# Performance work log

Hardware: AMD Instinct MI355X
Metric: run time of the kernel (lower is better)

Reference implementation:

```python
import jax, jax.numpy as jnp
import numpy as np

B, S, R, C_Q, C_KV, H, C_A = 1, 128, 256, 256, 256, 8, 32


def setup_inputs() -> dict:
    key = jax.random.key(0)
    ks = jax.random.split(key, 11)
    scale = 0.02
    q = jax.random.normal(ks[0], (B, S, R, C_Q), jnp.float32)
    kv = jax.random.normal(ks[1], (B, S, R, C_KV), jnp.float32)
    bias = jax.random.normal(ks[2], (B, 1, R, R, H), jnp.float32)
    bias_mask = jax.random.randint(ks[3], (B, S, R), 0, 2).astype(jnp.float32)
    w_q = jax.random.normal(ks[4], (C_Q, H, C_A), jnp.float32) * scale
    w_k = jax.random.normal(ks[5], (C_KV, H, C_A), jnp.float32) * scale
    w_v = jax.random.normal(ks[6], (C_KV, H, C_A), jnp.float32) * scale
    w_g = jax.random.normal(ks[7], (C_Q, H, C_A), jnp.float32) * scale
    b_g = jax.random.normal(ks[8], (H, C_A), jnp.float32) * scale
    w_o = jax.random.normal(ks[9], (H, C_A, C_Q), jnp.float32) * scale
    b_o = jax.random.normal(ks[10], (C_Q,), jnp.float32) * scale
    return {"q": q, "kv": kv, "bias": bias, "bias_mask": bias_mask,
            "w_q": w_q, "w_k": w_k, "w_v": w_v, "w_g": w_g, "b_g": b_g,
            "w_o": w_o, "b_o": b_o}


def reference(q, kv, bias, bias_mask, w_q, w_k, w_v, w_g, b_g, w_o, b_o):
    # q, kv: [B, S, R, C]; attention over residue dim R within each row s.
    c_a = w_q.shape[-1]
    normsize = 1.0 / jnp.sqrt(jnp.asarray(c_a, q.dtype))
    Q = jnp.einsum('bsqc,chd->bsqhd', q, w_q) * normsize  # [B,S,R,H,Ca]
    K = jnp.einsum('bskc,chd->bskhd', kv, w_k)
    V = jnp.einsum('bskc,chd->bskhd', kv, w_v)
    # affinity: [B,S,Q,K,H]
    AT = jnp.einsum('bsqhd,bskhd->bsqkh', Q, K)
    mask_bias = (bias_mask[:, :, None, :, None] - 1.0) * 1e9  # [B,S,1,K,1]
    AT = AT + bias + mask_bias
    AT = jax.nn.softmax(AT, axis=-2)  # softmax over K
    O = jnp.einsum('bsqkh,bskhd->bsqhd', AT, V)
    G = jax.nn.sigmoid(jnp.einsum('bsqc,chd->bsqhd', q, w_g) + b_g)
    O = O * G
    out = jnp.einsum('bsqhd,hdc->bsqc', O, w_o) + b_o  # [B,S,R,C_Q]
    return out
```

## Files before the change

### kernel.cpp

```cpp
#include <hip/hip_runtime.h>

typedef __bf16 bf16;
typedef __bf16 bf16x8 __attribute__((ext_vector_type(8)));
typedef float  f32x4  __attribute__((ext_vector_type(4)));
typedef unsigned int u32;

#define MFMA16(a, b, c) __builtin_amdgcn_mfma_f32_16x16x32_bf16((a), (b), (c), 0, 0, 0)


typedef __attribute__((address_space(3))) u32 lds_u32;
typedef const __attribute__((address_space(1))) u32 glob_u32;
__device__ __forceinline__ void gll16(const void* g, void* l) {
    __builtin_amdgcn_global_load_lds((glob_u32*)g, (lds_u32*)l, 16, 0, 0);
}

__global__ __launch_bounds__(256) void prep_kernel(
    const float* __restrict__ q, const float* __restrict__ kv,
    const float* __restrict__ bias,
    const float* __restrict__ w_q, const float* __restrict__ w_k,
    const float* __restrict__ w_v, const float* __restrict__ w_g,
    const float* __restrict__ w_o,
    bf16* __restrict__ qbf, bf16* __restrict__ kvbf, float* __restrict__ biasT,
    bf16* __restrict__ Wqg, bf16* __restrict__ Wkv, bf16* __restrict__ Wo)
{
    const float norm = 0.17677669529663687f;
    const int gid = blockIdx.x * 256 + threadIdx.x;
    const int gsz = gridDim.x * 256;

    for (int u = gid; u < 2097152; u += gsz) {
        const float* src; bf16* dst;
        if (u < 1048576) { src = q + (size_t)u * 8;            dst = qbf  + (size_t)u * 8; }
        else             { src = kv + (size_t)(u - 1048576)*8; dst = kvbf + (size_t)(u - 1048576)*8; }
        float4 x0 = *(const float4*)(src);
        float4 x1 = *(const float4*)(src + 4);
        bf16x8 t;
        t[0]=(bf16)x0.x; t[1]=(bf16)x0.y; t[2]=(bf16)x0.z; t[3]=(bf16)x0.w;
        t[4]=(bf16)x1.x; t[5]=(bf16)x1.y; t[6]=(bf16)x1.z; t[7]=(bf16)x1.w;
        *(bf16x8*)dst = t;
    }
    for (int u = gid; u < 524288; u += gsz) {
        int h = u >> 16, qq = (u >> 8) & 255, kk = u & 255;
        biasT[u] = bias[(((qq << 8) + kk) << 3) + h];
    }
    for (int u = gid; u < 131072; u += gsz) {
        int n = u >> 8, k = u & 255;
        float v = (n < 256) ? w_q[k * 256 + n] * norm : w_g[k * 256 + (n - 256)];
        Wqg[u] = (bf16)v;
    }
    for (int u = gid; u < 131072; u += gsz) {
        int n = u >> 8, k = u & 255;
        float v = (n < 256) ? w_k[k * 256 + n] : w_v[k * 256 + (n - 256)];
        Wkv[u] = (bf16)v;
    }
    for (int u = gid; u < 65536; u += gsz) {
        int n = u >> 8, k = u & 255;
        Wo[u] = (bf16)w_o[k * 256 + n];
    }
}

template<bool F32OUT>
__device__ __forceinline__ void gemm_core(
    const bf16* __restrict__ A, const bf16* __restrict__ Bw,
    bf16* __restrict__ Cb, float* __restrict__ Cf, const float* __restrict__ bo,
    int m0, int n0, int ntot)
{
    __shared__ __align__(16) bf16 As[128 * 32];
    __shared__ __align__(16) bf16 Bs[128 * 32];

    const int tid  = threadIdx.x;
    const int lane = tid & 63, wave = tid >> 6;
    const int quad = lane >> 4, lc = lane & 15;
    const int wr = wave >> 1, wc = wave & 1;

    const int r0 = tid >> 2, p0 = tid & 3;
    const int c1 = tid + 256;
    const int r1 = (c1 & 255) >> 2, p1 = c1 & 3;
    const bf16* gA0 = A  + (size_t)(m0 + r0) * 256 + p0 * 8;
    const bf16* gA1 = A  + (size_t)(m0 + 64 + r0) * 256 + p0 * 8;
    const bf16* gB0 = Bw + (size_t)(n0 + r0) * 256 + p0 * 8;
    const bf16* gB1 = Bw + (size_t)(n0 + 64 + r0) * 256 + p0 * 8;
    bf16* lA0 = As + tid * 8;
    bf16* lA1 = As + (tid + 256) * 8;
    bf16* lB0 = Bs + tid * 8;
    bf16* lB1 = Bs + (tid + 256) * 8;
    (void)r1; (void)p1;

    f32x4 acc[4][4];
    #pragma unroll
    for (int i = 0; i < 4; ++i)
        #pragma unroll
        for (int j = 0; j < 4; ++j) acc[i][j] = f32x4{0.f, 0.f, 0.f, 0.f};

    #pragma unroll 1
    for (int kb = 0; kb < 8; ++kb) {
        const int ko = kb * 32;
        gll16(gA0 + ko, lA0);
        gll16(gA1 + ko, lA1);
        gll16(gB0 + ko, lB0);
        gll16(gB1 + ko, lB1);
        __syncthreads();

        bf16x8 aF[4], bF[4];
        #pragma unroll
        for (int mt = 0; mt < 4; ++mt)
            aF[mt] = *(const bf16x8*)(As + (wr * 64 + mt * 16 + lc) * 32 + quad * 8);
        #pragma unroll
        for (int nt = 0; nt < 4; ++nt)
            bF[nt] = *(const bf16x8*)(Bs + (wc * 64 + nt * 16 + lc) * 32 + quad * 8);
        #pragma unroll
        for (int mt = 0; mt < 4; ++mt)
            #pragma unroll
            for (int nt = 0; nt < 4; ++nt)
                acc[mt][nt] = MFMA16(aF[mt], bF[nt], acc[mt][nt]);
        __syncthreads();
    }

    #pragma unroll
    for (int mt = 0; mt < 4; ++mt) {
        #pragma unroll
        for (int nt = 0; nt < 4; ++nt) {
            const int row = m0 + wr * 64 + mt * 16 + quad * 4;
            const int col = n0 + wc * 64 + nt * 16 + lc;
            if (F32OUT) {
                float b = bo[col];
                #pragma unroll
                for (int rr = 0; rr < 4; ++rr)
                    Cf[(size_t)(row + rr) * ntot + col] = acc[mt][nt][rr] + b;
            } else {
                #pragma unroll
                for (int rr = 0; rr < 4; ++rr)
                    Cb[(size_t)(row + rr) * ntot + col] = (bf16)acc[mt][nt][rr];
            }
        }
    }
}


__global__ __launch_bounds__(256) void proj_kernel(
    const bf16* __restrict__ qbf, const bf16* __restrict__ kvbf,
    const bf16* __restrict__ Wqg, const bf16* __restrict__ Wkv,
    bf16* __restrict__ QG, bf16* __restrict__ KV)
{
    int bid = blockIdx.x;
    bool sel = bid >= 1024;
    int b = sel ? bid - 1024 : bid;
    int m0 = (b >> 2) * 128, n0 = (b & 3) * 128;
    gemm_core<false>(sel ? kvbf : qbf, sel ? Wkv : Wqg,
                     sel ? KV : QG, nullptr, nullptr, m0, n0, 512);
}

__global__ __launch_bounds__(256) void outproj_kernel(
    const bf16* __restrict__ OG, const bf16* __restrict__ Wo,
    const float* __restrict__ bo, float* __restrict__ out)
{
    int b = blockIdx.x;
    int m0 = (b >> 1) * 128, n0 = (b & 1) * 128;
    gemm_core<true>(OG, Wo, nullptr, out, bo, m0, n0, 256);
}

#define A_OFF_MASK 0
#define A_OFF_K    1024
#define A_OFF_VT   21504
#define A_OFF_P    38400
#define A_LDS_TOT  (38400 + 4 * 16 * 264 * 2)

__global__ __launch_bounds__(256) void attn_kernel(
    const bf16* __restrict__ QG, const bf16* __restrict__ KV,
    const float* __restrict__ biasT, const float* __restrict__ bias_mask,
    const float* __restrict__ b_g, bf16* __restrict__ OG)
{
    __shared__ __align__(16) char smem[A_LDS_TOT];
    float* maskadd = (float*)(smem + A_OFF_MASK);
    bf16*  Ks      = (bf16*)(smem + A_OFF_K);
    bf16*  Vt      = (bf16*)(smem + A_OFF_VT);

    const int tid  = threadIdx.x;
    const int wave = tid >> 6, lane = tid & 63;
    const int quad = lane >> 4, lc = lane & 15;
    const int h = blockIdx.x & 7;
    const int s = blockIdx.x >> 3;

    maskadd[tid] = (bias_mask[s * 256 + tid] - 1.0f) * 1e9f;
    {
        const bf16* kvrow = KV + (size_t)(s * 256 + tid) * 512 + h * 32;
        #pragma unroll
        for (int j = 0; j < 4; ++j)
            *(bf16x8*)(Ks + tid * 40 + j * 8) = *(const bf16x8*)(kvrow + j * 8);
        bf16x8 vx[4];
        #pragma unroll
        for (int j = 0; j < 4; ++j) vx[j] = *(const bf16x8*)(kvrow + 256 + j * 8);
        #pragma unroll
        for (int d = 0; d < 32; ++d)
            Vt[d * 264 + tid] = vx[d >> 3][d & 7];
    }
    __syncthreads();

    bf16* P = (bf16*)(smem + A_OFF_P) + wave * (16 * 264);
    const bf16* qgbase = QG + (size_t)(s * 256) * 512 + h * 32;

    #pragma unroll 1
    for (int p = 0; p < 4; ++p) {
        const int q0 = (wave * 4 + p) * 16;

        bf16x8 qf = *(const bf16x8*)(qgbase + (size_t)(q0 + lc) * 512 + quad * 8);

        f32x4 sc[16];
        #pragma unroll
        for (int kt = 0; kt < 16; ++kt) {
            bf16x8 kf = *(const bf16x8*)(Ks + (kt * 16 + lc) * 40 + quad * 8);
            f32x4 z = {0.f, 0.f, 0.f, 0.f};
            sc[kt] = MFMA16(qf, kf, z);
        }

        const float* bT = biasT + (((size_t)h * 256 + q0 + quad * 4) << 8);
        float sum[4] = {0.f, 0.f, 0.f, 0.f};
        #pragma unroll
        for (int kt = 0; kt < 16; ++kt) {
            float mv = maskadd[kt * 16 + lc];
            #pragma unroll
            for (int rr = 0; rr < 4; ++rr) {
                float e = __expf(sc[kt][rr] + bT[rr * 256 + kt * 16 + lc] + mv);
                sc[kt][rr] = e;
                sum[rr] += e;
            }
        }
        #pragma unroll
        for (int rr = 0; rr < 4; ++rr) {
            #pragma unroll
            for (int off = 8; off; off >>= 1) sum[rr] += __shfl_xor(sum[rr], off, 64);
        }
        float inv[4];
        #pragma unroll
        for (int rr = 0; rr < 4; ++rr) inv[rr] = 1.0f / sum[rr];

        #pragma unroll
        for (int kt = 0; kt < 16; ++kt)
            #pragma unroll
            for (int rr = 0; rr < 4; ++rr)
                P[(quad * 4 + rr) * 264 + kt * 16 + lc] = (bf16)(sc[kt][rr] * inv[rr]);

        f32x4 o0 = {0.f,0.f,0.f,0.f}, o1 = {0.f,0.f,0.f,0.f};
        #pragma unroll
        for (int ks = 0; ks < 8; ++ks) {
            bf16x8 pf = *(const bf16x8*)(P + lc * 264 + ks * 32 + quad * 8);
            bf16x8 v0 = *(const bf16x8*)(Vt + lc * 264 + ks * 32 + quad * 8);
            bf16x8 v1 = *(const bf16x8*)(Vt + (16 + lc) * 264 + ks * 32 + quad * 8);
            o0 = MFMA16(pf, v0, o0);
            o1 = MFMA16(pf, v1, o1);
        }

        const bf16* gbase = QG + (size_t)(s * 256) * 512 + 256 + h * 32;
        size_t obase = ((size_t)(s * 256 + q0 + quad * 4)) * 256 + h * 32;
        #pragma unroll
        for (int nt = 0; nt < 2; ++nt) {
            f32x4 ov = nt ? o1 : o0;
            float bg = b_g[h * 32 + nt * 16 + lc];
            #pragma unroll
            for (int rr = 0; rr < 4; ++rr) {
                float gp = (float)gbase[(size_t)(q0 + quad * 4 + rr) * 512 + nt * 16 + lc] + bg;
                float g = 1.0f / (1.0f + __expf(-gp));
                OG[obase + (size_t)rr * 256 + nt * 16 + lc] = (bf16)(ov[rr] * g);
            }
        }
    }
}

extern "C" void kernel_launch(void* const* d_in, const int* in_sizes, int n_in,
                              void* d_out, int out_size, void* d_ws, size_t ws_size,
                              hipStream_t stream)
{
    (void)in_sizes; (void)n_in; (void)out_size; (void)ws_size;
    const float* q    = (const float*)d_in[0];
    const float* kv   = (const float*)d_in[1];
    const float* bias = (const float*)d_in[2];
    const float* mask = (const float*)d_in[3];
    const float* w_q  = (const float*)d_in[4];
    const float* w_k  = (const float*)d_in[5];
    const float* w_v  = (const float*)d_in[6];
    const float* w_g  = (const float*)d_in[7];
    const float* b_g  = (const float*)d_in[8];
    const float* w_o  = (const float*)d_in[9];
    const float* b_o  = (const float*)d_in[10];
    float* out = (float*)d_out;

    char* ws = (char*)d_ws;
    bf16*  qbf   = (bf16*)(ws + 0);
    bf16*  kvbf  = (bf16*)(ws + 16777216);
    bf16*  QG    = (bf16*)(ws + 33554432);
    bf16*  KV    = (bf16*)(ws + 67108864);
    float* biasT = (float*)(ws + 100663296);
    bf16*  Wqg   = (bf16*)(ws + 102760448);
    bf16*  Wkv   = (bf16*)(ws + 103022592);
    bf16*  Wo    = (bf16*)(ws + 103284736);
    bf16*  OG    = qbf;

    prep_kernel<<<1024, 256, 0, stream>>>(q, kv, bias, w_q, w_k, w_v, w_g, w_o,
                                          qbf, kvbf, biasT, Wqg, Wkv, Wo);
    proj_kernel<<<2048, 256, 0, stream>>>(qbf, kvbf, Wqg, Wkv, QG, KV);
    attn_kernel<<<1024, 256, 0, stream>>>(QG, KV, biasT, mask, b_g, OG);
    outproj_kernel<<<512, 256, 0, stream>>>(OG, Wo, b_o, out);
}
```

Before: 232.4 us.

## Fuse fp32-to-bf16 input cast into projection GEMM and restructure attention loads

Drops the separate fp32-to-bf16 conversion pass over q and kv; the projection GEMM now reads the fp32 activations and converts them in registers. The GEMMs switch from LDS-staged tiles to direct global-to-register fragment loads with 512-thread blocks and wider N tiles. In attention, K is read straight from global memory instead of LDS, and bias plus mask are pre-laid out so they can seed the MFMA accumulator. P is written to LDS with vectorized stores, with the V column order permuted to match. Without LDS staging, global operand traffic per block rises, and register pressure goes up.

```diff
diff --git a/kernel.cpp b/kernel.cpp
--- a/kernel.cpp
+++ b/kernel.cpp
@@ -3,176 +3,120 @@
 typedef __bf16 bf16;
 typedef __bf16 bf16x8 __attribute__((ext_vector_type(8)));
 typedef float  f32x4  __attribute__((ext_vector_type(4)));
-typedef unsigned int u32;
 
 #define MFMA16(a, b, c) __builtin_amdgcn_mfma_f32_16x16x32_bf16((a), (b), (c), 0, 0, 0)
 
 
-typedef __attribute__((address_space(3))) u32 lds_u32;
-typedef const __attribute__((address_space(1))) u32 glob_u32;
-__device__ __forceinline__ void gll16(const void* g, void* l) {
-    __builtin_amdgcn_global_load_lds((glob_u32*)g, (lds_u32*)l, 16, 0, 0);
-}
-
 __global__ __launch_bounds__(256) void prep_kernel(
-    const float* __restrict__ q, const float* __restrict__ kv,
     const float* __restrict__ bias,
     const float* __restrict__ w_q, const float* __restrict__ w_k,
     const float* __restrict__ w_v, const float* __restrict__ w_g,
     const float* __restrict__ w_o,
-    bf16* __restrict__ qbf, bf16* __restrict__ kvbf, float* __restrict__ biasT,
+    float* __restrict__ biasC,
     bf16* __restrict__ Wqg, bf16* __restrict__ Wkv, bf16* __restrict__ Wo)
 {
     const float norm = 0.17677669529663687f;
     const int gid = blockIdx.x * 256 + threadIdx.x;
     const int gsz = gridDim.x * 256;
-
-    for (int u = gid; u < 2097152; u += gsz) {
-        const float* src; bf16* dst;
-        if (u < 1048576) { src = q + (size_t)u * 8;            dst = qbf  + (size_t)u * 8; }
-        else             { src = kv + (size_t)(u - 1048576)*8; dst = kvbf + (size_t)(u - 1048576)*8; }
-        float4 x0 = *(const float4*)(src);
-        float4 x1 = *(const float4*)(src + 4);
-        bf16x8 t;
-        t[0]=(bf16)x0.x; t[1]=(bf16)x0.y; t[2]=(bf16)x0.z; t[3]=(bf16)x0.w;
-        t[4]=(bf16)x1.x; t[5]=(bf16)x1.y; t[6]=(bf16)x1.z; t[7]=(bf16)x1.w;
-        *(bf16x8*)dst = t;
-    }
-    for (int u = gid; u < 524288; u += gsz) {
-        int h = u >> 16, qq = (u >> 8) & 255, kk = u & 255;
-        biasT[u] = bias[(((qq << 8) + kk) << 3) + h];
-    }
-    for (int u = gid; u < 131072; u += gsz) {
-        int n = u >> 8, k = u & 255;
-        float v = (n < 256) ? w_q[k * 256 + n] * norm : w_g[k * 256 + (n - 256)];
-        Wqg[u] = (bf16)v;
-    }
-    for (int u = gid; u < 131072; u += gsz) {
-        int n = u >> 8, k = u & 255;
-        float v = (n < 256) ? w_k[k * 256 + n] : w_v[k * 256 + (n - 256)];
-        Wkv[u] = (bf16)v;
-    }
-    for (int u = gid; u < 65536; u += gsz) {
-        int n = u >> 8, k = u & 255;
-        Wo[u] = (bf16)w_o[k * 256 + n];
-    }
-}
-
-template<bool F32OUT>
-__device__ __forceinline__ void gemm_core(
-    const bf16* __restrict__ A, const bf16* __restrict__ Bw,
-    bf16* __restrict__ Cb, float* __restrict__ Cf, const float* __restrict__ bo,
-    int m0, int n0, int ntot)
-{
-    __shared__ __align__(16) bf16 As[128 * 32];
-    __shared__ __align__(16) bf16 Bs[128 * 32];
-
-    const int tid  = threadIdx.x;
-    const int lane = tid & 63, wave = tid >> 6;
+    for (int u = gid; u < 851968; u += gsz) {
+        if (u < 131072) {
+            int n = u >> 8, k = u & 255;
+            float v = (n < 256) ? w_q[k * 256 + n] * norm : w_g[k * 256 + (n - 256)];
+            Wqg[u] = (bf16)v;
+        } else if (u < 262144) {
+            int i = u - 131072;
+            int n = i >> 8, k = i & 255;
+            float v = (n < 256) ? w_k[k * 256 + n] : w_v[k * 256 + (n - 256)];
+            Wkv[i] = (bf16)v;
+        } else if (u < 327680) {
+            int i = u - 262144;
+            int n = i >> 8, k = i & 255;
+            Wo[i] = (bf16)w_o[k * 256 + n];
+        } else {
+            int o = u - 327680;
+            int rr = o & 3, k = (o >> 2) & 255, quad = (o >> 10) & 3;
+            int t = (o >> 12) & 15, h = o >> 16;
+            int q = t * 16 + quad * 4 + rr;
+            biasC[o] = bias[((q << 8) + k) * 8 + h];
+        }
+    }
+}
+
+__global__ __launch_bounds__(512, 2) void proj_kernel(
+    const float* __restrict__ qin, const float* __restrict__ kvin,
+    const bf16* __restrict__ Wqg, const bf16* __restrict__ Wkv,
+    bf16* __restrict__ QG, bf16* __restrict__ KV)
+{
+    const int b = blockIdx.x;
+    const bool sel = b >= 256;
+    const float* A  = sel ? kvin : qin;
+    const bf16*  Bw = sel ? Wkv : Wqg;
+    bf16*        Cc = sel ? KV : QG;
+    const int m0 = (b & 255) * 128;
+
+    const int tid = threadIdx.x, wave = tid >> 6, lane = tid & 63;
     const int quad = lane >> 4, lc = lane & 15;
-    const int wr = wave >> 1, wc = wave & 1;
-
-    const int r0 = tid >> 2, p0 = tid & 3;
-    const int c1 = tid + 256;
-    const int r1 = (c1 & 255) >> 2, p1 = c1 & 3;
-    const bf16* gA0 = A  + (size_t)(m0 + r0) * 256 + p0 * 8;
-    const bf16* gA1 = A  + (size_t)(m0 + 64 + r0) * 256 + p0 * 8;
-    const bf16* gB0 = Bw + (size_t)(n0 + r0) * 256 + p0 * 8;
-    const bf16* gB1 = Bw + (size_t)(n0 + 64 + r0) * 256 + p0 * 8;
-    bf16* lA0 = As + tid * 8;
-    bf16* lA1 = As + (tid + 256) * 8;
-    bf16* lB0 = Bs + tid * 8;
-    bf16* lB1 = Bs + (tid + 256) * 8;
-    (void)r1; (void)p1;
-
-    f32x4 acc[4][4];
+    const int wr = wave & 1, wc = wave >> 1;
+
+    const float* ar[4];
+    #pragma unroll
+    for (int mt = 0; mt < 4; ++mt)
+        ar[mt] = A + (size_t)(m0 + wr * 64 + mt * 16 + lc) * 256 + quad * 8;
+    const bf16* br[8];
+    #pragma unroll
+    for (int nt = 0; nt < 8; ++nt)
+        br[nt] = Bw + (size_t)(wc * 128 + nt * 16 + lc) * 256 + quad * 8;
+
+    f32x4 acc[4][8];
     #pragma unroll
     for (int i = 0; i < 4; ++i)
         #pragma unroll
-        for (int j = 0; j < 4; ++j) acc[i][j] = f32x4{0.f, 0.f, 0.f, 0.f};
-
-    #pragma unroll 1
+        for (int j = 0; j < 8; ++j) acc[i][j] = f32x4{0.f, 0.f, 0.f, 0.f};
+
+    #pragma unroll 2
     for (int kb = 0; kb < 8; ++kb) {
         const int ko = kb * 32;
-        gll16(gA0 + ko, lA0);
-        gll16(gA1 + ko, lA1);
-        gll16(gB0 + ko, lB0);
-        gll16(gB1 + ko, lB1);
-        __syncthreads();
-
-        bf16x8 aF[4], bF[4];
+        bf16x8 aF[4], bF[8];
+        #pragma unroll
+        for (int mt = 0; mt < 4; ++mt) {
+            float4 x0 = *(const float4*)(ar[mt] + ko);
+            float4 x1 = *(const float4*)(ar[mt] + ko + 4);
+            bf16x8 t;
+            t[0]=(bf16)x0.x; t[1]=(bf16)x0.y; t[2]=(bf16)x0.z; t[3]=(bf16)x0.w;
+            t[4]=(bf16)x1.x; t[5]=(bf16)x1.y; t[6]=(bf16)x1.z; t[7]=(bf16)x1.w;
+            aF[mt] = t;
+        }
+        #pragma unroll
+        for (int nt = 0; nt < 8; ++nt) bF[nt] = *(const bf16x8*)(br[nt] + ko);
         #pragma unroll
         for (int mt = 0; mt < 4; ++mt)
-            aF[mt] = *(const bf16x8*)(As + (wr * 64 + mt * 16 + lc) * 32 + quad * 8);
-        #pragma unroll
-        for (int nt = 0; nt < 4; ++nt)
-            bF[nt] = *(const bf16x8*)(Bs + (wc * 64 + nt * 16 + lc) * 32 + quad * 8);
-        #pragma unroll
-        for (int mt = 0; mt < 4; ++mt)
-            #pragma unroll
-            for (int nt = 0; nt < 4; ++nt)
+            #pragma unroll
+            for (int nt = 0; nt < 8; ++nt)
                 acc[mt][nt] = MFMA16(aF[mt], bF[nt], acc[mt][nt]);
-        __syncthreads();
-    }
-
-    #pragma unroll
-    for (int mt = 0; mt < 4; ++mt) {
-        #pragma unroll
-        for (int nt = 0; nt < 4; ++nt) {
+    }
+
+    #pragma unroll
+    for (int mt = 0; mt < 4; ++mt)
+        #pragma unroll
+        for (int nt = 0; nt < 8; ++nt) {
             const int row = m0 + wr * 64 + mt * 16 + quad * 4;
-            const int col = n0 + wc * 64 + nt * 16 + lc;
-            if (F32OUT) {
-                float b = bo[col];
-                #pragma unroll
-                for (int rr = 0; rr < 4; ++rr)
-                    Cf[(size_t)(row + rr) * ntot + col] = acc[mt][nt][rr] + b;
-            } else {
-                #pragma unroll
-                for (int rr = 0; rr < 4; ++rr)
-                    Cb[(size_t)(row + rr) * ntot + col] = (bf16)acc[mt][nt][rr];
-            }
-        }
-    }
-}
-
-
-__global__ __launch_bounds__(256) void proj_kernel(
-    const bf16* __restrict__ qbf, const bf16* __restrict__ kvbf,
-    const bf16* __restrict__ Wqg, const bf16* __restrict__ Wkv,
-    bf16* __restrict__ QG, bf16* __restrict__ KV)
-{
-    int bid = blockIdx.x;
-    bool sel = bid >= 1024;
-    int b = sel ? bid - 1024 : bid;
-    int m0 = (b >> 2) * 128, n0 = (b & 3) * 128;
-    gemm_core<false>(sel ? kvbf : qbf, sel ? Wkv : Wqg,
-                     sel ? KV : QG, nullptr, nullptr, m0, n0, 512);
-}
-
-__global__ __launch_bounds__(256) void outproj_kernel(
-    const bf16* __restrict__ OG, const bf16* __restrict__ Wo,
-    const float* __restrict__ bo, float* __restrict__ out)
-{
-    int b = blockIdx.x;
-    int m0 = (b >> 1) * 128, n0 = (b & 1) * 128;
-    gemm_core<true>(OG, Wo, nullptr, out, bo, m0, n0, 256);
-}
-
-#define A_OFF_MASK 0
-#define A_OFF_K    1024
-#define A_OFF_VT   21504
-#define A_OFF_P    38400
-#define A_LDS_TOT  (38400 + 4 * 16 * 264 * 2)
-
-__global__ __launch_bounds__(256) void attn_kernel(
+            const int col = wc * 128 + nt * 16 + lc;
+            #pragma unroll
+            for (int rr = 0; rr < 4; ++rr)
+                Cc[(size_t)(row + rr) * 512 + col] = (bf16)acc[mt][nt][rr];
+        }
+}
+
+#define A_LDS_TOT (1024 + 16896 + 33792)
+
+__global__ __launch_bounds__(256, 3) void attn_kernel(
     const bf16* __restrict__ QG, const bf16* __restrict__ KV,
-    const float* __restrict__ biasT, const float* __restrict__ bias_mask,
+    const float* __restrict__ biasC, const float* __restrict__ bias_mask,
     const float* __restrict__ b_g, bf16* __restrict__ OG)
 {
     __shared__ __align__(16) char smem[A_LDS_TOT];
-    float* maskadd = (float*)(smem + A_OFF_MASK);
-    bf16*  Ks      = (bf16*)(smem + A_OFF_K);
-    bf16*  Vt      = (bf16*)(smem + A_OFF_VT);
+    float* maskadd = (float*)(smem);
+    bf16*  Vt      = (bf16*)(smem + 1024);
 
     const int tid  = threadIdx.x;
     const int wave = tid >> 6, lane = tid & 63;
@@ -182,48 +126,47 @@
 
     maskadd[tid] = (bias_mask[s * 256 + tid] - 1.0f) * 1e9f;
     {
-        const bf16* kvrow = KV + (size_t)(s * 256 + tid) * 512 + h * 32;
-        #pragma unroll
-        for (int j = 0; j < 4; ++j)
-            *(bf16x8*)(Ks + tid * 40 + j * 8) = *(const bf16x8*)(kvrow + j * 8);
+        const bf16* kvrow = KV + (size_t)(s * 256 + tid) * 512 + 256 + h * 32;
         bf16x8 vx[4];
         #pragma unroll
-        for (int j = 0; j < 4; ++j) vx[j] = *(const bf16x8*)(kvrow + 256 + j * 8);
+        for (int j = 0; j < 4; ++j) vx[j] = *(const bf16x8*)(kvrow + j * 8);
+        const int kp = (tid & 15) * 16 + (tid >> 4);
         #pragma unroll
         for (int d = 0; d < 32; ++d)
-            Vt[d * 264 + tid] = vx[d >> 3][d & 7];
+            Vt[d * 264 + kp] = vx[d >> 3][d & 7];
     }
     __syncthreads();
 
-    bf16* P = (bf16*)(smem + A_OFF_P) + wave * (16 * 264);
-    const bf16* qgbase = QG + (size_t)(s * 256) * 512 + h * 32;
+    bf16* P = (bf16*)(smem + 17920) + wave * (16 * 264);
+    const bf16* qbase = QG + (size_t)(s * 256) * 512 + h * 32;
+    const bf16* gbase = qbase + 256;
+    const bf16* kbase = KV + (size_t)(s * 256) * 512 + h * 32;
 
     #pragma unroll 1
     for (int p = 0; p < 4; ++p) {
         const int q0 = (wave * 4 + p) * 16;
-
-        bf16x8 qf = *(const bf16x8*)(qgbase + (size_t)(q0 + lc) * 512 + quad * 8);
-
+        bf16x8 qf = *(const bf16x8*)(qbase + (size_t)(q0 + lc) * 512 + quad * 8);
+
+        const float* bC = biasC + (size_t)(((h * 16 + (q0 >> 4)) * 4 + quad) * 256) * 4;
         f32x4 sc[16];
         #pragma unroll
         for (int kt = 0; kt < 16; ++kt) {
-            bf16x8 kf = *(const bf16x8*)(Ks + (kt * 16 + lc) * 40 + quad * 8);
-            f32x4 z = {0.f, 0.f, 0.f, 0.f};
-            sc[kt] = MFMA16(qf, kf, z);
-        }
-
-        const float* bT = biasT + (((size_t)h * 256 + q0 + quad * 4) << 8);
+            bf16x8 kf = *(const bf16x8*)(kbase + (size_t)(kt * 16 + lc) * 512 + quad * 8);
+            f32x4 ci = *(const f32x4*)(bC + (kt * 16 + lc) * 4);
+            const float mv = maskadd[kt * 16 + lc];
+            ci[0] += mv; ci[1] += mv; ci[2] += mv; ci[3] += mv;
+            sc[kt] = MFMA16(qf, kf, ci);
+        }
+
         float sum[4] = {0.f, 0.f, 0.f, 0.f};
         #pragma unroll
-        for (int kt = 0; kt < 16; ++kt) {
-            float mv = maskadd[kt * 16 + lc];
+        for (int kt = 0; kt < 16; ++kt)
             #pragma unroll
             for (int rr = 0; rr < 4; ++rr) {
-                float e = __expf(sc[kt][rr] + bT[rr * 256 + kt * 16 + lc] + mv);
+                float e = __expf(sc[kt][rr]);
                 sc[kt][rr] = e;
                 sum[rr] += e;
             }
-        }
         #pragma unroll
         for (int rr = 0; rr < 4; ++rr) {
             #pragma unroll
@@ -234,10 +177,17 @@
         for (int rr = 0; rr < 4; ++rr) inv[rr] = 1.0f / sum[rr];
 
         #pragma unroll
-        for (int kt = 0; kt < 16; ++kt)
-            #pragma unroll
-            for (int rr = 0; rr < 4; ++rr)
-                P[(quad * 4 + rr) * 264 + kt * 16 + lc] = (bf16)(sc[kt][rr] * inv[rr]);
+        for (int rr = 0; rr < 4; ++rr) {
+            bf16x8 w0, w1;
+            #pragma unroll
+            for (int j = 0; j < 8; ++j) {
+                w0[j] = (bf16)(sc[j][rr] * inv[rr]);
+                w1[j] = (bf16)(sc[8 + j][rr] * inv[rr]);
+            }
+            bf16* pr = P + (quad * 4 + rr) * 264 + lc * 16;
+            *(bf16x8*)(pr)     = w0;
+            *(bf16x8*)(pr + 8) = w1;
+        }
 
         f32x4 o0 = {0.f,0.f,0.f,0.f}, o1 = {0.f,0.f,0.f,0.f};
         #pragma unroll
@@ -249,7 +199,6 @@
             o1 = MFMA16(pf, v1, o1);
         }
 
-        const bf16* gbase = QG + (size_t)(s * 256) * 512 + 256 + h * 32;
         size_t obase = ((size_t)(s * 256 + q0 + quad * 4)) * 256 + h * 32;
         #pragma unroll
         for (int nt = 0; nt < 2; ++nt) {
@@ -263,6 +212,58 @@
             }
         }
     }
+}
+
+__global__ __launch_bounds__(512, 2) void outproj_kernel(
+    const bf16* __restrict__ OG, const bf16* __restrict__ Wo,
+    const float* __restrict__ bo, float* __restrict__ out)
+{
+    const int m0 = blockIdx.x * 128;
+    const int tid = threadIdx.x, wave = tid >> 6, lane = tid & 63;
+    const int quad = lane >> 4, lc = lane & 15;
+    const int wr = wave & 1, wc = wave >> 1;
+
+    const bf16* ar[4];
+    #pragma unroll
+    for (int mt = 0; mt < 4; ++mt)
+        ar[mt] = OG + (size_t)(m0 + wr * 64 + mt * 16 + lc) * 256 + quad * 8;
+    const bf16* br[4];
+    #pragma unroll
+    for (int nt = 0; nt < 4; ++nt)
+        br[nt] = Wo + (size_t)(wc * 64 + nt * 16 + lc) * 256 + quad * 8;
+
+    f32x4 acc[4][4];
+    #pragma unroll
+    for (int i = 0; i < 4; ++i)
+        #pragma unroll
+        for (int j = 0; j < 4; ++j) acc[i][j] = f32x4{0.f, 0.f, 0.f, 0.f};
+
+    #pragma unroll 2
+    for (int kb = 0; kb < 8; ++kb) {
+        const int ko = kb * 32;
+        bf16x8 aF[4], bF[4];
+        #pragma unroll
+        for (int mt = 0; mt < 4; ++mt) aF[mt] = *(const bf16x8*)(ar[mt] + ko);
+        #pragma unroll
+        for (int nt = 0; nt < 4; ++nt) bF[nt] = *(const bf16x8*)(br[nt] + ko);
+        #pragma unroll
+        for (int mt = 0; mt < 4; ++mt)
+            #pragma unroll
+            for (int nt = 0; nt < 4; ++nt)
+                acc[mt][nt] = MFMA16(aF[mt], bF[nt], acc[mt][nt]);
+    }
+
+    #pragma unroll
+    for (int mt = 0; mt < 4; ++mt)
+        #pragma unroll
+        for (int nt = 0; nt < 4; ++nt) {
+            const int row = m0 + wr * 64 + mt * 16 + quad * 4;
+            const int col = wc * 64 + nt * 16 + lc;
+            const float b = bo[col];
+            #pragma unroll
+            for (int rr = 0; rr < 4; ++rr)
+                out[(size_t)(row + rr) * 256 + col] = acc[mt][nt][rr] + b;
+        }
 }
 
 extern "C" void kernel_launch(void* const* d_in, const int* in_sizes, int n_in,
@@ -284,19 +285,17 @@
     float* out = (float*)d_out;
 
     char* ws = (char*)d_ws;
-    bf16*  qbf   = (bf16*)(ws + 0);
-    bf16*  kvbf  = (bf16*)(ws + 16777216);
-    bf16*  QG    = (bf16*)(ws + 33554432);
-    bf16*  KV    = (bf16*)(ws + 67108864);
-    float* biasT = (float*)(ws + 100663296);
-    bf16*  Wqg   = (bf16*)(ws + 102760448);
-    bf16*  Wkv   = (bf16*)(ws + 103022592);
-    bf16*  Wo    = (bf16*)(ws + 103284736);
-    bf16*  OG    = qbf;
-
-    prep_kernel<<<1024, 256, 0, stream>>>(q, kv, bias, w_q, w_k, w_v, w_g, w_o,
-                                          qbf, kvbf, biasT, Wqg, Wkv, Wo);
-    proj_kernel<<<2048, 256, 0, stream>>>(qbf, kvbf, Wqg, Wkv, QG, KV);
-    attn_kernel<<<1024, 256, 0, stream>>>(QG, KV, biasT, mask, b_g, OG);
-    outproj_kernel<<<512, 256, 0, stream>>>(OG, Wo, b_o, out);
-}
+    bf16*  QG    = (bf16*)(ws + 0);
+    bf16*  KV    = (bf16*)(ws + 33554432);
+    bf16*  OG    = (bf16*)(ws + 67108864);
+    float* biasC = (float*)(ws + 83886080);
+    bf16*  Wqg   = (bf16*)(ws + 85983232);
+    bf16*  Wkv   = (bf16*)(ws + 86245376);
+    bf16*  Wo    = (bf16*)(ws + 86507520);
+
+    prep_kernel<<<416, 256, 0, stream>>>(bias, w_q, w_k, w_v, w_g, w_o,
+                                         biasC, Wqg, Wkv, Wo);
+    proj_kernel<<<512, 512, 0, stream>>>(q, kv, Wqg, Wkv, QG, KV);
+    attn_kernel<<<1024, 256, 0, stream>>>(QG, KV, biasC, mask, b_g, OG);
+    outproj_kernel<<<256, 512, 0, stream>>>(OG, Wo, b_o, out);
+}
```

Result: slower. 370.1 us (+59.3%).
